# Kernel tuning notes

Hardware: AMD Instinct MI355X
Metric: run time of the kernel (lower is better)

Reference implementation:

```python
import jax, jax.numpy as jnp
import numpy as np

HID = 128
NUM_LAYERS = 3
B = 256
ND, ED, SD = 16384, 65536, 131072
NP_, EP, SP = 131072, 524288, 524288


def setup_inputs():
    key = jax.random.key(0)
    ks = jax.random.split(key, 40)
    r = lambda i, sh: jax.random.normal(ks[i], sh, jnp.float32) * 0.05
    ri = lambda i, sh, hi: jax.random.randint(ks[i], sh, 0, hi, jnp.int32)
    return {
        'drug_x': r(0, (ND, 78)),
        'prot_x': r(1, (NP_, 70)),
        'd_feature': r(2, (B, HID)),
        'p_feature': r(3, (B, HID)),
        'drug_edge_index': ri(4, (2, ED), ND),
        'drug_batch': jnp.sort(ri(5, (ND,), B)),
        'drug_sub_node': ri(6, (SD,), ND),
        'drug_sub_ind': ri(7, (SD,), ND),
        'prot_edge_index': ri(8, (2, EP), NP_),
        'prot_batch': jnp.sort(ri(9, (NP_,), B)),
        'prot_sub_node': ri(10, (SP,), NP_),
        'prot_sub_ind': ri(11, (SP,), NP_),
        'enc_Wd': r(12, (78, HID)), 'enc_bd': r(13, (HID,)),
        'enc_Wp': r(14, (70, HID)), 'enc_bp': r(15, (HID,)),
        'convW_d': r(16, (NUM_LAYERS, HID, HID)), 'convb_d': r(17, (NUM_LAYERS, HID)),
        'convW_p': r(18, (NUM_LAYERS, HID, HID)), 'convb_p': r(19, (NUM_LAYERS, HID)),
        'bng_d': jnp.ones((NUM_LAYERS, HID), jnp.float32), 'bnb_d': jnp.zeros((NUM_LAYERS, HID), jnp.float32),
        'bng_p': jnp.ones((NUM_LAYERS, HID), jnp.float32), 'bnb_p': jnp.zeros((NUM_LAYERS, HID), jnp.float32),
        'vn_emb_d': r(20, (HID,)), 'vn_emb_p': r(21, (HID,)),
        'vnW_d': r(22, (NUM_LAYERS - 1, HID, HID)), 'vnb_d': r(23, (NUM_LAYERS - 1, HID)),
        'vnW_p': r(24, (NUM_LAYERS - 1, HID, HID)), 'vnb_p': r(25, (NUM_LAYERS - 1, HID)),
        'mlpd1_W': r(26, (2 * HID, HID)), 'mlpd1_b': r(27, (HID,)),
        'mlpd1_g': jnp.ones((HID,), jnp.float32), 'mlpd1_be': jnp.zeros((HID,), jnp.float32),
        'mlpp1_W': r(28, (2 * HID, HID)), 'mlpp1_b': r(29, (HID,)),
        'mlpp1_g': jnp.ones((HID,), jnp.float32), 'mlpp1_be': jnp.zeros((HID,), jnp.float32),
    }


def _bn(x, g, b):
    # training-mode batch norm (batch statistics)
    m = jnp.mean(x, 0)
    v = jnp.var(x, 0)
    return (x - m) * jax.lax.rsqrt(v + 1e-5) * g + b


def _seg_mean(x, ids, n):
    s = jax.ops.segment_sum(x, ids, num_segments=n)
    c = jax.ops.segment_sum(jnp.ones((x.shape[0],), x.dtype), ids, num_segments=n)
    return s / jnp.maximum(c, 1.0)[:, None]


def _gcn(h, W, b, ei, n):
    # PyG GCNConv: sym-normalized A+I, then linear
    src, dst = ei[0], ei[1]
    hw = h @ W
    deg = jax.ops.segment_sum(jnp.ones((src.shape[0],), h.dtype), dst, num_segments=n) + 1.0
    nrm = jax.lax.rsqrt(deg)
    msg = hw[src] * (nrm[src] * nrm[dst])[:, None]  # [E, HID]
    return jax.ops.segment_sum(msg, dst, num_segments=n) + hw * (nrm * nrm)[:, None] + b


def _forward(fl, ints):
    (drug_x, prot_x, d_feature, p_feature, enc_Wd, enc_bd, enc_Wp, enc_bp,
     convW_d, convb_d, convW_p, convb_p, bng_d, bnb_d, bng_p, bnb_p,
     vn_emb_d, vn_emb_p, vnW_d, vnb_d, vnW_p, vnb_p,
     mlpd1_W, mlpd1_b, mlpd1_g, mlpd1_be, mlpp1_W, mlpp1_b, mlpp1_g, mlpp1_be) = fl
    (d_ei, d_batch, d_sn, d_si, p_ei, p_batch, p_sn, p_si) = ints
    Nd, Npn = drug_x.shape[0], prot_x.shape[0]
    Bn = d_feature.shape[0]
    hd = drug_x @ enc_Wd + enc_bd
    hp = prot_x @ enc_Wp + enc_bp
    # virtual node init: learned embedding + pretrained fingerprint feature
    vx_d = vn_emb_d[None, :] + d_feature  # [B, HID]
    vx_p = vn_emb_p[None, :] + p_feature
    for i in range(NUM_LAYERS):
        # virtual-node broadcast -> GCN -> BN -> ReLU (dropout off / eval)
        hd = _gcn(hd + vx_d[d_batch], convW_d[i], convb_d[i], d_ei, Nd)
        hp = _gcn(hp + vx_p[p_batch], convW_p[i], convb_p[i], p_ei, Npn)
        hd = jax.nn.relu(_bn(hd, bng_d[i], bnb_d[i]))
        hp = jax.nn.relu(_bn(hp, bng_p[i], bnb_p[i]))
        # k-hop subgraph structure extraction (scatter_mean back to nodes)
        hd_struct = _seg_mean(hd[d_sn], d_si, Nd)
        hp_struct = _seg_mean(hp[p_sn], p_si, Npn)
        if i < NUM_LAYERS - 1:
            vx_d = vx_d + jax.nn.relu((jax.ops.segment_sum(hd_struct, d_batch, num_segments=Bn) + vx_d) @ vnW_d[i] + vnb_d[i])
            vx_p = vx_p + jax.nn.relu((jax.ops.segment_sum(hp_struct, p_batch, num_segments=Bn) + vx_p) @ vnW_p[i] + vnb_p[i])
    # cross-modal sync: broadcast pooled drug info onto protein nodes & vice versa
    sync_drug = hp_struct + _seg_mean(hd_struct, d_batch, Bn)[p_batch]  # [Np, HID]
    sync_prot = hd_struct + _seg_mean(hp_struct, p_batch, Bn)[d_batch]  # [Nd, HID]
    final_drug = _bn(jnp.concatenate([_seg_mean(sync_prot, d_batch, Bn), d_feature], 1) @ mlpd1_W + mlpd1_b, mlpd1_g, mlpd1_be)
    final_prot = _bn(jnp.concatenate([_seg_mean(sync_drug, p_batch, Bn), p_feature], 1) @ mlpp1_W + mlpp1_b, mlpp1_g, mlpp1_be)
    return final_drug, final_prot


def reference(drug_x, prot_x, d_feature, p_feature, drug_edge_index, drug_batch,
              drug_sub_node, drug_sub_ind, prot_edge_index, prot_batch,
              prot_sub_node, prot_sub_ind, enc_Wd, enc_bd, enc_Wp, enc_bp,
              convW_d, convb_d, convW_p, convb_p, bng_d, bnb_d, bng_p, bnb_p,
              vn_emb_d, vn_emb_p, vnW_d, vnb_d, vnW_p, vnb_p,
              mlpd1_W, mlpd1_b, mlpd1_g, mlpd1_be, mlpp1_W, mlpp1_b, mlpp1_g, mlpp1_be):
    fl = (drug_x, prot_x, d_feature, p_feature, enc_Wd, enc_bd, enc_Wp, enc_bp,
          convW_d, convb_d, convW_p, convb_p, bng_d, bnb_d, bng_p, bnb_p,
          vn_emb_d, vn_emb_p, vnW_d, vnb_d, vnW_p, vnb_p,
          mlpd1_W, mlpd1_b, mlpd1_g, mlpd1_be, mlpp1_W, mlpp1_b, mlpp1_g, mlpp1_be)
    ints = (drug_edge_index, drug_batch, drug_sub_node, drug_sub_ind,
            prot_edge_index, prot_batch, prot_sub_node, prot_sub_ind)
    return _forward(fl, ints)
```

## Files before the change

### kernel.cpp

```cpp
#include <hip/hip_runtime.h>
#include <cstdint>
#include <cstddef>

#define HID 128
#define HB 1024

using bf16x8 = __attribute__((ext_vector_type(8))) short;
using f32x4v = __attribute__((ext_vector_type(4))) float;

static __device__ __forceinline__ unsigned short f2b(float x) {
  unsigned int u = __float_as_uint(x);
  unsigned int r = u + 0x7FFFu + ((u >> 16) & 1u);
  return (unsigned short)(r >> 16);
}
static __device__ __forceinline__ float b2f(unsigned short h) {
  return __uint_as_float(((unsigned int)h) << 16);
}
static __device__ __forceinline__ float4 b2f4(ushort4 h) {
  return make_float4(b2f(h.x), b2f(h.y), b2f(h.z), b2f(h.w));
}

static __device__ __forceinline__ int lowerb(const int* __restrict__ a, int n, int v) {
  int lo = 0, hi = n;
  while (lo < hi) { int m = (lo + hi) >> 1; if (a[m] < v) lo = m + 1; else hi = m; }
  return lo;
}

__global__ __launch_bounds__(256)
void k_prep1(const int* p_dst, int EP, int* deg_p, const int* d_dst, int ED, int* deg_d,
             const int* p_si, int SP, int* scnt_p, const int* d_si, int SD, int* scnt_d,
             const float* convW_d, const float* convW_p,
             const float* enc_Wd, const float* enc_Wp,
             unsigned short* WhiAll, unsigned short* WloAll,
             const float* emb_d, const float* d_feat, float* vx_d,
             const float* emb_p, const float* p_feat, float* vx_p, int vhalf) {
  const int b = blockIdx.x;
  const int tid = threadIdx.x;
  if (b < 4 * HB) {
    const int seg = b & 3, lb = b >> 2;
    const int stride = HB * 256;
    const int* idx = seg == 0 ? p_dst : seg == 1 ? d_dst : seg == 2 ? p_si : d_si;
    int* cnt = seg == 0 ? deg_p : seg == 1 ? deg_d : seg == 2 ? scnt_p : scnt_d;
    const int n = seg == 0 ? EP : seg == 1 ? ED : seg == 2 ? SP : SD;
    for (int i = lb * 256 + tid; i < n; i += stride) atomicAdd(&cnt[idx[i]], 1);
  } else if (b < 4 * HB + 256) {
    const int lb = b - 4 * HB;
    const int seg = lb >> 5;
    const float* W;
    int K;
    if (seg < 3) { W = convW_d + (size_t)seg * HID * HID; K = 128; }
    else if (seg < 6) { W = convW_p + (size_t)(seg - 3) * HID * HID; K = 128; }
    else if (seg == 6) { W = enc_Wd; K = 78; }
    else { W = enc_Wp; K = 70; }
    unsigned short* Whi = WhiAll + (size_t)seg * HID * HID;
    unsigned short* Wlo = WloAll + (size_t)seg * HID * HID;
    for (int i = (lb & 31) * 256 + tid; i < HID * HID; i += 32 * 256) {
      const int c = i >> 7, k = i & 127;
      const float v = (k < K) ? W[k * HID + c] : 0.f;
      const unsigned short hi = f2b(v);
      Whi[i] = hi;
      Wlo[i] = f2b(v - b2f(hi));
    }
  } else {
    const int lb = b - (4 * HB + 256);
    for (int i = lb * 256 + tid; i < 2 * vhalf; i += 128 * 256) {
      if (i < vhalf) vx_d[i] = emb_d[i & (HID - 1)] + d_feat[i];
      else { const int j = i - vhalf; vx_p[j] = emb_p[j & (HID - 1)] + p_feat[j]; }
    }
  }
}

__global__ void k_nrm_nb(const int* deg_d, float* nrm_d, int ND,
                         const int* deg_p, float* nrm_p, int NP,
                         const int* d_batch, float* nb_d,
                         const int* p_batch, float* nb_p, int B) {
  const int stride = gridDim.x * blockDim.x;
  const int total = ND + NP + 2 * B;
  for (int i = blockIdx.x * blockDim.x + threadIdx.x; i < total; i += stride) {
    if (i < ND) nrm_d[i] = rsqrtf((float)deg_d[i] + 1.0f);
    else if (i < ND + NP) { const int j = i - ND; nrm_p[j] = rsqrtf((float)deg_p[j] + 1.0f); }
    else if (i < ND + NP + B) {
      const int b = i - ND - NP;
      nb_d[b] = (float)(lowerb(d_batch, ND, b + 1) - lowerb(d_batch, ND, b));
    } else {
      const int b = i - ND - NP - B;
      nb_p[b] = (float)(lowerb(p_batch, NP, b + 1) - lowerb(p_batch, NP, b));
    }
  }
}

__global__ __launch_bounds__(256)
void k_scan1_all(const int* c0, int* r0, int n0, int nb0,
                 const int* c1, int* r1, int n1, int nb1,
                 const int* c2, int* r2, int n2, int nb2,
                 const int* c3, int* r3, int n3, int nb3, int* aux) {
  __shared__ int sh[256];
  int b = blockIdx.x, seg = 0;
  if (b >= nb0) { b -= nb0; seg = 1; }
  if (seg == 1 && b >= nb1) { b -= nb1; seg = 2; }
  if (seg == 2 && b >= nb2) { b -= nb2; seg = 3; }
  const int* cnt = seg == 0 ? c0 : seg == 1 ? c1 : seg == 2 ? c2 : c3;
  int* row = seg == 0 ? r0 : seg == 1 ? r1 : seg == 2 ? r2 : r3;
  const int n = seg == 0 ? n0 : seg == 1 ? n1 : seg == 2 ? n2 : n3;
  const int tid = threadIdx.x;
  const int base = b * 1024 + tid * 4;
  int v0 = base + 0 < n ? cnt[base + 0] : 0;
  int v1 = base + 1 < n ? cnt[base + 1] : 0;
  int v2 = base + 2 < n ? cnt[base + 2] : 0;
  int v3 = base + 3 < n ? cnt[base + 3] : 0;
  const int s = v0 + v1 + v2 + v3;
  sh[tid] = s;
  __syncthreads();
  for (int o = 1; o < 256; o <<= 1) {
    const int t = (tid >= o) ? sh[tid - o] : 0;
    __syncthreads();
    sh[tid] += t;
    __syncthreads();
  }
  int excl = sh[tid] - s;
  if (tid == 255) aux[seg * 256 + b] = sh[255];
  if (base + 0 < n) row[base + 0] = excl; excl += v0;
  if (base + 1 < n) row[base + 1] = excl; excl += v1;
  if (base + 2 < n) row[base + 2] = excl; excl += v2;
  if (base + 3 < n) row[base + 3] = excl;
}

__global__ __launch_bounds__(256)
void k_scan2_all(int* aux, int nb0, int nb1, int nb2, int nb3) {
  __shared__ int sh[256];
  const int seg = blockIdx.x;
  const int nb = seg == 0 ? nb0 : seg == 1 ? nb1 : seg == 2 ? nb2 : nb3;
  int* a = aux + seg * 256;
  const int tid = threadIdx.x;
  const int v = tid < nb ? a[tid] : 0;
  sh[tid] = v;
  __syncthreads();
  for (int o = 1; o < 256; o <<= 1) {
    const int t = (tid >= o) ? sh[tid - o] : 0;
    __syncthreads();
    sh[tid] += t;
    __syncthreads();
  }
  if (tid < nb) a[tid] = sh[tid] - v;
}

__global__ __launch_bounds__(256)
void k_scan3_all(int* r0, int n0, int nb0, int t0, int* r1, int n1, int nb1, int t1,
                 int* r2, int n2, int nb2, int t2, int* r3, int n3, int nb3, int t3,
                 const int* aux) {
  int b = blockIdx.x, seg = 0;
  if (b >= nb0) { b -= nb0; seg = 1; }
  if (seg == 1 && b >= nb1) { b -= nb1; seg = 2; }
  if (seg == 2 && b >= nb2) { b -= nb2; seg = 3; }
  int* row = seg == 0 ? r0 : seg == 1 ? r1 : seg == 2 ? r2 : r3;
  const int n = seg == 0 ? n0 : seg == 1 ? n1 : seg == 2 ? n2 : n3;
  const int total = seg == 0 ? t0 : seg == 1 ? t1 : seg == 2 ? t2 : t3;
  const int add = aux[seg * 256 + b];
  const int base = b * 1024 + threadIdx.x * 4;
  #pragma unroll
  for (int k = 0; k < 4; ++k)
    if (base + k < n) row[base + k] += add;
  if (b == 0 && threadIdx.x == 0) row[n] = total;
}

__global__ void k_fill_all(const int* p_src, const int* p_dst, const int* rowE_p, int* curE_p,
                           int* colE_p, int EP,
                           const int* d_src, const int* d_dst, const int* rowE_d, int* curE_d,
                           int* colE_d, int ED,
                           const int* p_sn, const int* p_si, const int* rowS_p, int* curS_p,
                           int* colS_p, int SP,
                           const int* d_sn, const int* d_si, const int* rowS_d, int* curS_d,
                           int* colS_d, int SD) {
  const int seg = blockIdx.x & 3;
  const int lb = blockIdx.x >> 2;
  const int stride = (gridDim.x >> 2) * blockDim.x;
  const int start = lb * blockDim.x + threadIdx.x;
  if (seg == 0) {
    for (int e = start; e < EP; e += stride) {
      const int d = p_dst[e];
      colE_p[rowE_p[d] + atomicAdd(&curE_p[d], 1)] = p_src[e];
    }
  } else if (seg == 1) {
    for (int e = start; e < ED; e += stride) {
      const int d = d_dst[e];
      colE_d[rowE_d[d] + atomicAdd(&curE_d[d], 1)] = d_src[e];
    }
  } else if (seg == 2) {
    for (int j = start; j < SP; j += stride) {
      const int t = p_si[j];
      colS_p[rowS_p[t] + atomicAdd(&curS_p[t], 1)] = p_sn[j];
    }
  } else {
    for (int j = start; j < SD; j += stride) {
      const int t = d_si[j];
      colS_d[rowS_d[t] + atomicAdd(&curS_d[t], 1)] = d_sn[j];
    }
  }
}

__global__ __launch_bounds__(256, 2)
void k_gemm_both(const unsigned short* Zhi0, const unsigned short* Zlo0,
                 const unsigned short* Whi0, const unsigned short* Wlo0,
                 unsigned short* G0, int nbk0,
                 const unsigned short* Zhi1, const unsigned short* Zlo1,
                 const unsigned short* Whi1, const unsigned short* Wlo1,
                 unsigned short* G1, float* stats_sl) {
  __shared__ unsigned short Bt[128 * 132];
  __shared__ float lstats[256];
  const int bid = blockIdx.x;
  const bool isP = bid >= nbk0;
  const int lb = isP ? bid - nbk0 : bid;
  const unsigned short* Zhi = isP ? Zhi1 : Zhi0;
  const unsigned short* Zlo = isP ? Zlo1 : Zlo0;
  const unsigned short* Wthi = isP ? Whi1 : Whi0;
  const unsigned short* Wtlo = isP ? Wlo1 : Wlo0;
  unsigned short* G = isP ? G1 : G0;
  const int slice = (isP ? 32 : 0) + (lb & 31);

  const int tid = threadIdx.x;
  const int w = tid >> 6;
  const int l = tid & 63;
  const int l15 = l & 15;
  const int kb = l >> 4;

  for (int i = tid; i < 128 * 16; i += 256) {
    const int c = i >> 4, k8 = i & 15;
    *(bf16x8*)(&Bt[c * 132 + k8 * 8]) = *(const bf16x8*)(Wthi + (size_t)c * 128 + k8 * 8);
  }
  lstats[tid] = 0.f;

  const int rbase = lb * 128 + w * 32 + l15;
  bf16x8 ahi[2][4], alo[2][4];
  #pragma unroll
  for (int rt = 0; rt < 2; ++rt)
    #pragma unroll
    for (int ks = 0; ks < 4; ++ks) {
      ahi[rt][ks] = *(const bf16x8*)(Zhi + (size_t)(rbase + rt * 16) * 128 + ks * 32 + kb * 8);
      alo[rt][ks] = *(const bf16x8*)(Zlo + (size_t)(rbase + rt * 16) * 128 + ks * 32 + kb * 8);
    }

  f32x4v acc[2][8];
  #pragma unroll
  for (int rt = 0; rt < 2; ++rt)
    #pragma unroll
    for (int ct = 0; ct < 8; ++ct)
      acc[rt][ct] = (f32x4v){0.f, 0.f, 0.f, 0.f};

  __syncthreads();
  #pragma unroll
  for (int ks = 0; ks < 4; ++ks) {
    #pragma unroll
    for (int ct = 0; ct < 8; ++ct) {
      const bf16x8 b = *(const bf16x8*)(&Bt[(ct * 16 + l15) * 132 + ks * 32 + kb * 8]);
      acc[0][ct] = __builtin_amdgcn_mfma_f32_16x16x32_bf16(ahi[0][ks], b, acc[0][ct], 0, 0, 0);
      acc[1][ct] = __builtin_amdgcn_mfma_f32_16x16x32_bf16(ahi[1][ks], b, acc[1][ct], 0, 0, 0);
      acc[0][ct] = __builtin_amdgcn_mfma_f32_16x16x32_bf16(alo[0][ks], b, acc[0][ct], 0, 0, 0);
      acc[1][ct] = __builtin_amdgcn_mfma_f32_16x16x32_bf16(alo[1][ks], b, acc[1][ct], 0, 0, 0);
    }
  }
  __syncthreads();

  for (int i = tid; i < 128 * 16; i += 256) {
    const int c = i >> 4, k8 = i & 15;
    *(bf16x8*)(&Bt[c * 132 + k8 * 8]) = *(const bf16x8*)(Wtlo + (size_t)c * 128 + k8 * 8);
  }
  __syncthreads();
  #pragma unroll
  for (int ks = 0; ks < 4; ++ks) {
    #pragma unroll
    for (int ct = 0; ct < 8; ++ct) {
      const bf16x8 b = *(const bf16x8*)(&Bt[(ct * 16 + l15) * 132 + ks * 32 + kb * 8]);
      acc[0][ct] = __builtin_amdgcn_mfma_f32_16x16x32_bf16(ahi[0][ks], b, acc[0][ct], 0, 0, 0);
      acc[1][ct] = __builtin_amdgcn_mfma_f32_16x16x32_bf16(ahi[1][ks], b, acc[1][ct], 0, 0, 0);
    }
  }

  float csum[8], csq[8];
  #pragma unroll
  for (int ct = 0; ct < 8; ++ct) { csum[ct] = 0.f; csq[ct] = 0.f; }
  #pragma unroll
  for (int rt = 0; rt < 2; ++rt) {
    const size_t grow = (size_t)lb * 128 + w * 32 + rt * 16 + (l >> 4) * 4;
    #pragma unroll
    for (int j = 0; j < 4; ++j) {
      unsigned short* gr = G + (grow + j) * 128 + l15;
      #pragma unroll
      for (int ct = 0; ct < 8; ++ct) {
        const float v = acc[rt][ct][j];
        gr[ct * 16] = f2b(v);
        csum[ct] += v;
        csq[ct] += v * v;
      }
    }
  }
  #pragma unroll
  for (int ct = 0; ct < 8; ++ct) {
    csum[ct] += __shfl_xor(csum[ct], 16);
    csum[ct] += __shfl_xor(csum[ct], 32);
    csq[ct] += __shfl_xor(csq[ct], 16);
    csq[ct] += __shfl_xor(csq[ct], 32);
  }
  if (l < 16) {
    #pragma unroll
    for (int ct = 0; ct < 8; ++ct) {
      atomicAdd(&lstats[ct * 16 + l], csum[ct]);
      atomicAdd(&lstats[128 + ct * 16 + l], csq[ct]);
    }
  }
  __syncthreads();
  atomicAdd(&stats_sl[(size_t)slice * 256 + tid], lstats[tid]);
}

__global__ __launch_bounds__(256, 2)
void k_gemm_enc_direct(const float* X0, int K0,
                       const unsigned short* Whi0, const unsigned short* Wlo0,
                       const float* bias0, unsigned short* G0, int nbk0,
                       const float* X1, int K1,
                       const unsigned short* Whi1, const unsigned short* Wlo1,
                       const float* bias1, unsigned short* G1) {
  __shared__ unsigned short Bt[128 * 132];
  const int bid = blockIdx.x;
  const bool isP = bid >= nbk0;
  const int lb = isP ? bid - nbk0 : bid;
  const float* X = isP ? X1 : X0;
  const int K = isP ? K1 : K0;
  const unsigned short* Wthi = isP ? Whi1 : Whi0;
  const unsigned short* Wtlo = isP ? Wlo1 : Wlo0;
  const float* bias = isP ? bias1 : bias0;
  unsigned short* G = isP ? G1 : G0;

  const int tid = threadIdx.x;
  const int w = tid >> 6;
  const int l = tid & 63;
  const int l15 = l & 15;
  const int kb = l >> 4;

  for (int i = tid; i < 128 * 16; i += 256) {
    const int c = i >> 4, k8 = i & 15;
    *(bf16x8*)(&Bt[c * 132 + k8 * 8]) = *(const bf16x8*)(Wthi + (size_t)c * 128 + k8 * 8);
  }

  const int rbase = lb * 128 + w * 32 + l15;
  bf16x8 ahi[2][4], alo[2][4];
  #pragma unroll
  for (int rt = 0; rt < 2; ++rt) {
    const float* xr = X + (size_t)(rbase + rt * 16) * K;
    #pragma unroll
    for (int ks = 0; ks < 4; ++ks) {
      #pragma unroll
      for (int j = 0; j < 8; ++j) {
        const int k = ks * 32 + kb * 8 + j;
        const float v = (k < K) ? xr[k] : 0.f;
        const unsigned short hi = f2b(v);
        ahi[rt][ks][j] = (short)hi;
        alo[rt][ks][j] = (short)f2b(v - b2f(hi));
      }
    }
  }

  f32x4v acc[2][8];
  #pragma unroll
  for (int rt = 0; rt < 2; ++rt)
    #pragma unroll
    for (int ct = 0; ct < 8; ++ct)
      acc[rt][ct] = (f32x4v){0.f, 0.f, 0.f, 0.f};

  __syncthreads();
  #pragma unroll
  for (int ks = 0; ks < 4; ++ks) {
    #pragma unroll
    for (int ct = 0; ct < 8; ++ct) {
      const bf16x8 b = *(const bf16x8*)(&Bt[(ct * 16 + l15) * 132 + ks * 32 + kb * 8]);
      acc[0][ct] = __builtin_amdgcn_mfma_f32_16x16x32_bf16(ahi[0][ks], b, acc[0][ct], 0, 0, 0);
      acc[1][ct] = __builtin_amdgcn_mfma_f32_16x16x32_bf16(ahi[1][ks], b, acc[1][ct], 0, 0, 0);
      acc[0][ct] = __builtin_amdgcn_mfma_f32_16x16x32_bf16(alo[0][ks], b, acc[0][ct], 0, 0, 0);
      acc[1][ct] = __builtin_amdgcn_mfma_f32_16x16x32_bf16(alo[1][ks], b, acc[1][ct], 0, 0, 0);
    }
  }
  __syncthreads();

  for (int i = tid; i < 128 * 16; i += 256) {
    const int c = i >> 4, k8 = i & 15;
    *(bf16x8*)(&Bt[c * 132 + k8 * 8]) = *(const bf16x8*)(Wtlo + (size_t)c * 128 + k8 * 8);
  }
  __syncthreads();
  #pragma unroll
  for (int ks = 0; ks < 4; ++ks) {
    #pragma unroll
    for (int ct = 0; ct < 8; ++ct) {
      const bf16x8 b = *(const bf16x8*)(&Bt[(ct * 16 + l15) * 132 + ks * 32 + kb * 8]);
      acc[0][ct] = __builtin_amdgcn_mfma_f32_16x16x32_bf16(ahi[0][ks], b, acc[0][ct], 0, 0, 0);
      acc[1][ct] = __builtin_amdgcn_mfma_f32_16x16x32_bf16(ahi[1][ks], b, acc[1][ct], 0, 0, 0);
    }
  }

  float bb[8];
  #pragma unroll
  for (int ct = 0; ct < 8; ++ct) bb[ct] = bias[ct * 16 + l15];
  #pragma unroll
  for (int rt = 0; rt < 2; ++rt) {
    const size_t grow = (size_t)lb * 128 + w * 32 + rt * 16 + (l >> 4) * 4;
    #pragma unroll
    for (int j = 0; j < 4; ++j) {
      unsigned short* gr = G + (grow + j) * 128 + l15;
      #pragma unroll
      for (int ct = 0; ct < 8; ++ct)
        gr[ct * 16] = f2b(acc[rt][ct][j] + bb[ct]);
    }
  }
}

__global__ __launch_bounds__(128)
void k_bn_scale_both(float* __restrict__ stats_sl,
                     const float* g0, const float* b0, float invN0, float* scsh0, float* zero0,
                     const float* g1, const float* b1, float invN1, float* scsh1, float* zero1,
                     int zn4) {
  const int seg = blockIdx.x;
  float* base = stats_sl + (size_t)seg * 32 * 256;
  const float* g = seg ? g1 : g0;
  const float* bb = seg ? b1 : b0;
  const float invN = seg ? invN1 : invN0;
  float* scsh = seg ? scsh1 : scsh0;
  float* zero = seg ? zero1 : zero0;
  const int c = threadIdx.x;
  float s = 0.f, ss = 0.f;
  for (int k = 0; k < 32; ++k) {
    s += base[(size_t)k * 256 + c];
    ss += base[(size_t)k * 256 + 128 + c];
    base[(size_t)k * 256 + c] = 0.f;
    base[(size_t)k * 256 + 128 + c] = 0.f;
  }
  const float m = s * invN;
  const float var = ss * invN - m * m;
  const float sc = g[c] * rsqrtf(var + 1e-5f);
  scsh[c] = sc;
  scsh[HID + c] = bb[c] - m * sc;
  const float4 z = {0.f, 0.f, 0.f, 0.f};
  for (int i = c; i < zn4; i += 128) ((float4*)zero)[i] = z;
}

template<bool HASF>
__global__ __launch_bounds__(256)
void k_agg_both(const int* rE0, const int* cE0, const unsigned short* G0,
                const float* scsh0, const int* bat0, const float* vx0, const float* nrm0,
                unsigned short* Zhi0, unsigned short* Zlo0, int nbk0,
                const int* rE1, const int* cE1, const unsigned short* G1,
                const float* scsh1, const int* bat1, const float* vx1, const float* nrm1,
                unsigned short* Zhi1, unsigned short* Zlo1) {
  const int bid = blockIdx.x;
  const bool isP = bid >= nbk0;
  const int lb = isP ? bid - nbk0 : bid;
  const int* rowp = isP ? rE1 : rE0;
  const int* colp = isP ? cE1 : cE0;
  const unsigned short* G = isP ? G1 : G0;
  const float* scsh = isP ? scsh1 : scsh0;
  const int* batch = isP ? bat1 : bat0;
  const float* vx = isP ? vx1 : vx0;
  const float* nrm = isP ? nrm1 : nrm0;
  unsigned short* Zhi = isP ? Zhi1 : Zhi0;
  unsigned short* Zlo = isP ? Zlo1 : Zlo0;

  const int tid = threadIdx.x;
  const int node = lb * 8 + (tid >> 5);
  const int c4 = tid & 31;
  float4 sc, shv;
  if constexpr (HASF) {
    sc = ((const float4*)scsh)[c4];
    shv = ((const float4*)(scsh + HID))[c4];
  }
  auto loadU = [&](int i) -> float4 {
    float4 v = b2f4(*(const ushort4*)(G + (size_t)i * HID + c4 * 4));
    if constexpr (HASF) {
      v.x = fmaxf(v.x * sc.x + shv.x, 0.f);
      v.y = fmaxf(v.y * sc.y + shv.y, 0.f);
      v.z = fmaxf(v.z * sc.z + shv.z, 0.f);
      v.w = fmaxf(v.w * sc.w + shv.w, 0.f);
    }
    const float4 u = *(const float4*)(vx + (size_t)batch[i] * HID + c4 * 4);
    v.x += u.x; v.y += u.y; v.z += u.z; v.w += u.w;
    return v;
  };
  const int lo = rowp[node], hi = rowp[node + 1];
  const float nv = nrm[node];
  const float s2 = nv * nv;
  float4 acc = loadU(node);
  acc.x *= s2; acc.y *= s2; acc.z *= s2; acc.w *= s2;
  int e = lo;
  for (; e + 4 <= hi; e += 4) {
    const int i0 = colp[e], i1 = colp[e + 1], i2 = colp[e + 2], i3 = colp[e + 3];
    const float w0 = nrm[i0] * nv, w1 = nrm[i1] * nv, w2 = nrm[i2] * nv, w3 = nrm[i3] * nv;
    const float4 v0 = loadU(i0);
    const float4 v1 = loadU(i1);
    const float4 v2 = loadU(i2);
    const float4 v3 = loadU(i3);
    acc.x += v0.x * w0 + v1.x * w1 + v2.x * w2 + v3.x * w3;
    acc.y += v0.y * w0 + v1.y * w1 + v2.y * w2 + v3.y * w3;
    acc.z += v0.z * w0 + v1.z * w1 + v2.z * w2 + v3.z * w3;
    acc.w += v0.w * w0 + v1.w * w1 + v2.w * w2 + v3.w * w3;
  }
  for (; e < hi; ++e) {
    const int i0 = colp[e];
    const float w = nrm[i0] * nv;
    const float4 v = loadU(i0);
    acc.x += v.x * w; acc.y += v.y * w; acc.z += v.z * w; acc.w += v.w * w;
  }
  ushort4 h, lo4;
  h.x = f2b(acc.x); lo4.x = f2b(acc.x - b2f(h.x));
  h.y = f2b(acc.y); lo4.y = f2b(acc.y - b2f(h.y));
  h.z = f2b(acc.z); lo4.z = f2b(acc.z - b2f(h.z));
  h.w = f2b(acc.w); lo4.w = f2b(acc.w - b2f(h.w));
  *(ushort4*)(Zhi + (size_t)node * HID + c4 * 4) = h;
  *(ushort4*)(Zlo + (size_t)node * HID + c4 * 4) = lo4;
}

__global__ __launch_bounds__(256)
void k_sub_pool_both(const int* rS0, const int* cS0, const unsigned short* G0, const float* scsh0,
                     const int* bat0, float* sumS0, int nbk0,
                     const int* rS1, const int* cS1, const unsigned short* G1, const float* scsh1,
                     const int* bat1, float* sumS1) {
  __shared__ float sh[8][HID];
  __shared__ int batl[8];
  const int bid = blockIdx.x;
  const bool isP = bid >= nbk0;
  const int lb = isP ? bid - nbk0 : bid;
  const int* rowp = isP ? rS1 : rS0;
  const int* colp = isP ? cS1 : cS0;
  const unsigned short* G = isP ? G1 : G0;
  const float* scsh = isP ? scsh1 : scsh0;
  const int* batch = isP ? bat1 : bat0;
  float* sumS = isP ? sumS1 : sumS0;

  const int tid = threadIdx.x;
  const int grp = tid >> 5;
  const int node = lb * 8 + grp;
  const int c4 = tid & 31;
  const float4 sc = ((const float4*)scsh)[c4];
  const float4 shv = ((const float4*)(scsh + HID))[c4];
  const int lo = rowp[node], hi = rowp[node + 1];
  float4 acc = {0.f, 0.f, 0.f, 0.f};
  int e = lo;
  for (; e + 4 <= hi; e += 4) {
    const int i0 = colp[e], i1 = colp[e + 1], i2 = colp[e + 2], i3 = colp[e + 3];
    const float4 v0 = b2f4(*(const ushort4*)(G + (size_t)i0 * HID + c4 * 4));
    const float4 v1 = b2f4(*(const ushort4*)(G + (size_t)i1 * HID + c4 * 4));
    const float4 v2 = b2f4(*(const ushort4*)(G + (size_t)i2 * HID + c4 * 4));
    const float4 v3 = b2f4(*(const ushort4*)(G + (size_t)i3 * HID + c4 * 4));
    acc.x += fmaxf(v0.x * sc.x + shv.x, 0.f) + fmaxf(v1.x * sc.x + shv.x, 0.f)
           + fmaxf(v2.x * sc.x + shv.x, 0.f) + fmaxf(v3.x * sc.x + shv.x, 0.f);
    acc.y += fmaxf(v0.y * sc.y + shv.y, 0.f) + fmaxf(v1.y * sc.y + shv.y, 0.f)
           + fmaxf(v2.y * sc.y + shv.y, 0.f) + fmaxf(v3.y * sc.y + shv.y, 0.f);
    acc.z += fmaxf(v0.z * sc.z + shv.z, 0.f) + fmaxf(v1.z * sc.z + shv.z, 0.f)
           + fmaxf(v2.z * sc.z + shv.z, 0.f) + fmaxf(v3.z * sc.z + shv.z, 0.f);
    acc.w += fmaxf(v0.w * sc.w + shv.w, 0.f) + fmaxf(v1.w * sc.w + shv.w, 0.f)
           + fmaxf(v2.w * sc.w + shv.w, 0.f) + fmaxf(v3.w * sc.w + shv.w, 0.f);
  }
  for (; e < hi; ++e) {
    const float4 v = b2f4(*(const ushort4*)(G + (size_t)colp[e] * HID + c4 * 4));
    acc.x += fmaxf(v.x * sc.x + shv.x, 0.f);
    acc.y += fmaxf(v.y * sc.y + shv.y, 0.f);
    acc.z += fmaxf(v.z * sc.z + shv.z, 0.f);
    acc.w += fmaxf(v.w * sc.w + shv.w, 0.f);
  }
  const float inv = 1.0f / fmaxf((float)(hi - lo), 1.0f);
  acc.x *= inv; acc.y *= inv; acc.z *= inv; acc.w *= inv;
  ((float4*)&sh[grp][0])[c4] = acc;
  if (tid < 8) batl[tid] = batch[lb * 8 + tid];
  __syncthreads();
  if (tid < HID) {
    int cur = batl[0];
    float a = 0.f;
    #pragma unroll
    for (int g = 0; g < 8; ++g) {
      if (batl[g] != cur) {
        atomicAdd(&sumS[(size_t)cur * HID + tid], a);
        a = 0.f;
        cur = batl[g];
      }
      a += sh[g][tid];
    }
    atomicAdd(&sumS[(size_t)cur * HID + tid], a);
  }
}

__global__ __launch_bounds__(128)
void k_vn_update_both(const float* ps0, float* vx0, const float* W0, const float* b0,
                      const float* ps1, float* vx1, const float* W1, const float* b1, int B) {
  const int gb = blockIdx.x;
  const bool isP = gb >= B;
  const int b = isP ? gb - B : gb;
  const float* pooledSum = isP ? ps1 : ps0;
  float* vx = isP ? vx1 : vx0;
  const float* W = isP ? W1 : W0;
  const float* bias = isP ? b1 : b0;
  const int c = threadIdx.x;
  __shared__ float xin[HID];
  xin[c] = pooledSum[(size_t)b * HID + c] + vx[(size_t)b * HID + c];
  __syncthreads();
  float acc = bias[c];
  #pragma unroll 8
  for (int k = 0; k < HID; k += 4) {
    const float4 x = *(const float4*)&xin[k];
    acc += x.x * W[k * HID + c] + x.y * W[(k + 1) * HID + c]
         + x.z * W[(k + 2) * HID + c] + x.w * W[(k + 3) * HID + c];
  }
  vx[(size_t)b * HID + c] += fmaxf(acc, 0.0f);
}

__global__ __launch_bounds__(128)
void k_final_A(const float* __restrict__ sum_Sd, const float* __restrict__ sum_Sp,
               const float* __restrict__ nb_d, const float* __restrict__ nb_p,
               float* __restrict__ A_d, float* __restrict__ A_p) {
  const int b = blockIdx.x, c = threadIdx.x;
  const float nd = nb_d[b], np_ = nb_p[b];
  const float md = sum_Sd[(size_t)b * HID + c] / fmaxf(nd, 1.f);
  const float mp = sum_Sp[(size_t)b * HID + c] / fmaxf(np_, 1.f);
  A_d[(size_t)b * HID + c] = md + (nd > 0.f ? mp : 0.f);
  A_p[(size_t)b * HID + c] = mp + (np_ > 0.f ? md : 0.f);
}

__global__ __launch_bounds__(128)
void k_final_mlp_both(const float* A0, const float* f0, const float* W0, const float* b0,
                      const float* A1, const float* f1, const float* W1, const float* b1,
                      float* __restrict__ fpre, int B) {
  const int gb = blockIdx.x;
  const bool isP = gb >= B;
  const int b = isP ? gb - B : gb;
  const float* A = isP ? A1 : A0;
  const float* feat = isP ? f1 : f0;
  const float* W = isP ? W1 : W0;
  const float* bias = isP ? b1 : b0;
  const int c = threadIdx.x;
  __shared__ float xin[2 * HID];
  xin[c] = A[(size_t)b * HID + c];
  xin[HID + c] = feat[(size_t)b * HID + c];
  __syncthreads();
  float acc = bias[c];
  #pragma unroll 8
  for (int k = 0; k < 2 * HID; k += 4) {
    const float4 x = *(const float4*)&xin[k];
    acc += x.x * W[k * HID + c] + x.y * W[(k + 1) * HID + c]
         + x.z * W[(k + 2) * HID + c] + x.w * W[(k + 3) * HID + c];
  }
  fpre[(size_t)gb * HID + c] = acc;
}

__global__ __launch_bounds__(256)
void k_bn_stats_both(const float* __restrict__ fpre, float* __restrict__ statsF, int B) {
  __shared__ float sh[2][256];
  const int seg = blockIdx.x >= 128 ? 1 : 0;
  const int lb = blockIdx.x - seg * 128;
  const float* X = fpre + (size_t)seg * B * HID;
  float* stats = statsF + seg * 256;
  const int tid = threadIdx.x;
  const int c = tid & (HID - 1);
  const int half = tid >> 7;
  float s = 0.f, ss = 0.f;
  for (int r = lb * 2 + half; r < B; r += 256) {
    const float v = X[(size_t)r * HID + c];
    s += v; ss += v * v;
  }
  sh[0][tid] = s; sh[1][tid] = ss;
  __syncthreads();
  if (tid < HID) {
    atomicAdd(&stats[c], sh[0][tid] + sh[0][tid + 128]);
    atomicAdd(&stats[HID + c], sh[1][tid] + sh[1][tid + 128]);
  }
}

__global__ void k_bn_apply_both(const float* __restrict__ fpre, float* __restrict__ out,
                                const float* __restrict__ statsF,
                                const float* g0, const float* b0,
                                const float* g1, const float* b1, int B, float invN) {
  const int stride = gridDim.x * blockDim.x;
  const int n4 = 2 * B * 32;
  for (int i = blockIdx.x * blockDim.x + threadIdx.x; i < n4; i += stride) {
    const int seg = i >= B * 32 ? 1 : 0;
    const int c4 = i & 31;
    const float* stats = statsF + seg * 256;
    const float4 m4 = ((const float4*)stats)[c4];
    const float4 q4 = ((const float4*)stats)[32 + c4];
    const float4 g4 = ((const float4*)(seg ? g1 : g0))[c4];
    const float4 b4 = ((const float4*)(seg ? b1 : b0))[c4];
    float4 v = ((const float4*)fpre)[i];
    float m, va;
    m = m4.x * invN; va = q4.x * invN - m * m; v.x = (v.x - m) * rsqrtf(va + 1e-5f) * g4.x + b4.x;
    m = m4.y * invN; va = q4.y * invN - m * m; v.y = (v.y - m) * rsqrtf(va + 1e-5f) * g4.y + b4.y;
    m = m4.z * invN; va = q4.z * invN - m * m; v.z = (v.z - m) * rsqrtf(va + 1e-5f) * g4.z + b4.z;
    m = m4.w * invN; va = q4.w * invN - m * m; v.w = (v.w - m) * rsqrtf(va + 1e-5f) * g4.w + b4.w;
    ((float4*)out)[i] = v;
  }
}

extern "C" void kernel_launch(void* const* d_in, const int* in_sizes, int n_in,
                              void* d_out, int out_size, void* d_ws, size_t ws_size,
                              hipStream_t stream) {
  const float* drug_x   = (const float*)d_in[0];
  const float* prot_x   = (const float*)d_in[1];
  const float* d_feat   = (const float*)d_in[2];
  const float* p_feat   = (const float*)d_in[3];
  const int*   d_ei     = (const int*)d_in[4];
  const int*   d_batch  = (const int*)d_in[5];
  const int*   d_sn     = (const int*)d_in[6];
  const int*   d_si     = (const int*)d_in[7];
  const int*   p_ei     = (const int*)d_in[8];
  const int*   p_batch  = (const int*)d_in[9];
  const int*   p_sn     = (const int*)d_in[10];
  const int*   p_si     = (const int*)d_in[11];
  const float* enc_Wd   = (const float*)d_in[12];
  const float* enc_bd   = (const float*)d_in[13];
  const float* enc_Wp   = (const float*)d_in[14];
  const float* enc_bp   = (const float*)d_in[15];
  const float* convW_d  = (const float*)d_in[16];
  const float* convW_p  = (const float*)d_in[18];
  const float* bng_d    = (const float*)d_in[20];
  const float* bnb_d    = (const float*)d_in[21];
  const float* bng_p    = (const float*)d_in[22];
  const float* bnb_p    = (const float*)d_in[23];
  const float* vn_emb_d = (const float*)d_in[24];
  const float* vn_emb_p = (const float*)d_in[25];
  const float* vnW_d    = (const float*)d_in[26];
  const float* vnb_d    = (const float*)d_in[27];
  const float* vnW_p    = (const float*)d_in[28];
  const float* vnb_p    = (const float*)d_in[29];
  const float* mlpd1_W  = (const float*)d_in[30];
  const float* mlpd1_b  = (const float*)d_in[31];
  const float* mlpd1_g  = (const float*)d_in[32];
  const float* mlpd1_be = (const float*)d_in[33];
  const float* mlpp1_W  = (const float*)d_in[34];
  const float* mlpp1_b  = (const float*)d_in[35];
  const float* mlpp1_g  = (const float*)d_in[36];
  const float* mlpp1_be = (const float*)d_in[37];

  const int ND = in_sizes[5];
  const int ED = in_sizes[4] / 2;
  const int SD = in_sizes[6];
  const int NP = in_sizes[9];
  const int EP = in_sizes[8] / 2;
  const int SP = in_sizes[10];
  const int B  = in_sizes[2] / HID;
  (void)n_in; (void)out_size; (void)ws_size;

  char* wsb = (char*)d_ws;
  size_t off = 0;
  auto alloc = [&](size_t bytes) -> void* {
    void* p = (void*)(wsb + off);
    off = (off + bytes + 255) & ~(size_t)255;
    return p;
  };
  unsigned short* Gp = (unsigned short*)alloc((size_t)NP * HID * 2);
  unsigned short* Zhi_p = (unsigned short*)alloc((size_t)NP * HID * 2);
  unsigned short* Zlo_p = (unsigned short*)alloc((size_t)NP * HID * 2);
  unsigned short* Gd = (unsigned short*)alloc((size_t)ND * HID * 2);
  unsigned short* Zhi_d = (unsigned short*)alloc((size_t)ND * HID * 2);
  unsigned short* Zlo_d = (unsigned short*)alloc((size_t)ND * HID * 2);
  unsigned short* WhiAll = (unsigned short*)alloc((size_t)8 * HID * HID * 2);
  unsigned short* WloAll = (unsigned short*)alloc((size_t)8 * HID * HID * 2);
  float* nrm_p = (float*)alloc((size_t)NP * 4);
  float* nrm_d = (float*)alloc((size_t)ND * 4);
  int* rowE_p = (int*)alloc((size_t)(NP + 1) * 4);
  int* rowE_d = (int*)alloc((size_t)(ND + 1) * 4);
  int* rowS_p = (int*)alloc((size_t)(NP + 1) * 4);
  int* rowS_d = (int*)alloc((size_t)(ND + 1) * 4);
  int* colE_p = (int*)alloc((size_t)EP * 4);
  int* colE_d = (int*)alloc((size_t)ED * 4);
  int* colS_p = (int*)alloc((size_t)SP * 4);
  int* colS_d = (int*)alloc((size_t)SD * 4);
  int* aux    = (int*)alloc(4 * 256 * 4);
  float* vx_d  = (float*)alloc((size_t)B * HID * 4);
  float* vx_p  = (float*)alloc((size_t)B * HID * 4);
  float* sum_Sd = (float*)alloc((size_t)B * HID * 4);
  float* sum_Sp = (float*)alloc((size_t)B * HID * 4);
  float* A_d   = (float*)alloc((size_t)B * HID * 4);
  float* A_p   = (float*)alloc((size_t)B * HID * 4);
  float* nb_d  = (float*)alloc((size_t)B * 4);
  float* nb_p  = (float*)alloc((size_t)B * 4);
  float* scsh_d = (float*)alloc(2 * HID * 4);
  float* scsh_p = (float*)alloc(2 * HID * 4);
  float* fpre  = (float*)alloc((size_t)2 * B * HID * 4);
  float* statsF = (float*)alloc(2 * 256 * 4);
  const size_t zstart = off;
  int* deg_p  = (int*)alloc((size_t)NP * 4);
  int* deg_d  = (int*)alloc((size_t)ND * 4);
  int* scnt_p = (int*)alloc((size_t)NP * 4);
  int* scnt_d = (int*)alloc((size_t)ND * 4);
  int* curE_p = (int*)alloc((size_t)NP * 4);
  int* curE_d = (int*)alloc((size_t)ND * 4);
  int* curS_p = (int*)alloc((size_t)NP * 4);
  int* curS_d = (int*)alloc((size_t)ND * 4);
  float* stats_sl = (float*)alloc((size_t)64 * 256 * 4);
  const size_t zend = off;

  const int* d_src = d_ei;  const int* d_dst = d_ei + ED;
  const int* p_src = p_ei;  const int* p_dst = p_ei + EP;

  hipMemsetAsync(wsb + zstart, 0, zend - zstart, stream);
  k_prep1<<<4 * HB + 256 + 128, 256, 0, stream>>>(
      p_dst, EP, deg_p, d_dst, ED, deg_d, p_si, SP, scnt_p, d_si, SD, scnt_d,
      convW_d, convW_p, enc_Wd, enc_Wp, WhiAll, WloAll,
      vn_emb_d, d_feat, vx_d, vn_emb_p, p_feat, vx_p, B * HID);
  k_nrm_nb<<<1024, 256, 0, stream>>>(deg_d, nrm_d, ND, deg_p, nrm_p, NP,
                                     d_batch, nb_d, p_batch, nb_p, B);
  const int nbP = (NP + 1023) / 1024, nbD = (ND + 1023) / 1024;
  k_scan1_all<<<2 * nbP + 2 * nbD, 256, 0, stream>>>(
      deg_p, rowE_p, NP, nbP, deg_d, rowE_d, ND, nbD,
      scnt_p, rowS_p, NP, nbP, scnt_d, rowS_d, ND, nbD, aux);
  k_scan2_all<<<4, 256, 0, stream>>>(aux, nbP, nbD, nbP, nbD);
  k_scan3_all<<<2 * nbP + 2 * nbD, 256, 0, stream>>>(
      rowE_p, NP, nbP, EP, rowE_d, ND, nbD, ED,
      rowS_p, NP, nbP, SP, rowS_d, ND, nbD, SD, aux);
  k_fill_all<<<4096, 256, 0, stream>>>(
      p_src, p_dst, rowE_p, curE_p, colE_p, EP,
      d_src, d_dst, rowE_d, curE_d, colE_d, ED,
      p_sn, p_si, rowS_p, curS_p, colS_p, SP,
      d_sn, d_si, rowS_d, curS_d, colS_d, SD);

  k_gemm_enc_direct<<<ND / 128 + NP / 128, 256, 0, stream>>>(
      drug_x, 78, WhiAll + (size_t)6 * HID * HID, WloAll + (size_t)6 * HID * HID,
      enc_bd, Gd, ND / 128,
      prot_x, 70, WhiAll + (size_t)7 * HID * HID, WloAll + (size_t)7 * HID * HID,
      enc_bp, Gp);

  for (int l = 0; l < 3; ++l) {
    if (l == 0)
      k_agg_both<false><<<ND / 8 + NP / 8, 256, 0, stream>>>(
          rowE_d, colE_d, Gd, nullptr, d_batch, vx_d, nrm_d, Zhi_d, Zlo_d, ND / 8,
          rowE_p, colE_p, Gp, nullptr, p_batch, vx_p, nrm_p, Zhi_p, Zlo_p);
    else
      k_agg_both<true><<<ND / 8 + NP / 8, 256, 0, stream>>>(
          rowE_d, colE_d, Gd, scsh_d, d_batch, vx_d, nrm_d, Zhi_d, Zlo_d, ND / 8,
          rowE_p, colE_p, Gp, scsh_p, p_batch, vx_p, nrm_p, Zhi_p, Zlo_p);
    k_gemm_both<<<ND / 128 + NP / 128, 256, 0, stream>>>(
        Zhi_d, Zlo_d, WhiAll + (size_t)l * HID * HID, WloAll + (size_t)l * HID * HID,
        Gd, ND / 128,
        Zhi_p, Zlo_p, WhiAll + (size_t)(3 + l) * HID * HID, WloAll + (size_t)(3 + l) * HID * HID,
        Gp, stats_sl);
    k_bn_scale_both<<<2, 128, 0, stream>>>(stats_sl,
        bng_d + l * HID, bnb_d + l * HID, 1.0f / (float)ND, scsh_d, sum_Sd,
        bng_p + l * HID, bnb_p + l * HID, 1.0f / (float)NP, scsh_p, sum_Sp,
        B * HID / 4);
    k_sub_pool_both<<<ND / 8 + NP / 8, 256, 0, stream>>>(
        rowS_d, colS_d, Gd, scsh_d, d_batch, sum_Sd, ND / 8,
        rowS_p, colS_p, Gp, scsh_p, p_batch, sum_Sp);
    if (l < 2)
      k_vn_update_both<<<2 * B, 128, 0, stream>>>(
          sum_Sd, vx_d, vnW_d + (size_t)l * HID * HID, vnb_d + l * HID,
          sum_Sp, vx_p, vnW_p + (size_t)l * HID * HID, vnb_p + l * HID, B);
  }

  k_final_A<<<B, 128, 0, stream>>>(sum_Sd, sum_Sp, nb_d, nb_p, A_d, A_p);
  k_final_mlp_both<<<2 * B, 128, 0, stream>>>(A_d, d_feat, mlpd1_W, mlpd1_b,
                                              A_p, p_feat, mlpp1_W, mlpp1_b, fpre, B);
  hipMemsetAsync(statsF, 0, 2 * 256 * 4, stream);
  k_bn_stats_both<<<256, 256, 0, stream>>>(fpre, statsF, B);
  k_bn_apply_both<<<128, 256, 0, stream>>>(fpre, (float*)d_out, statsF,
                                           mlpd1_g, mlpd1_be, mlpp1_g, mlpp1_be,
                                           B, 1.0f / (float)B);
}
```

Before: 628.7 us.

## Partition histogram and CSR fill atomics by XCD node range; fuse final mean into MLP

The degree-count and CSR-fill kernels now map each block to one of eight XCDs by its low block-index bits. Each block only handles keys in that XCD's slice of the node range, so atomics on a given counter stay within one XCD's L2 and avoid cross-XCD coherence traffic. In exchange every XCD group re-reads the full index arrays, and the grids are smaller. Separately, the k_final_A kernel is folded into k_final_mlp_both, which removes one launch and the A_d/A_p buffers.

```diff
diff --git a/kernel.cpp b/kernel.cpp
--- a/kernel.cpp
+++ b/kernel.cpp
@@ -3,7 +3,6 @@
 #include <cstddef>
 
 #define HID 128
-#define HB 1024
 
 using bf16x8 = __attribute__((ext_vector_type(8))) short;
 using f32x4v = __attribute__((ext_vector_type(4))) float;
@@ -29,6 +28,7 @@
 __global__ __launch_bounds__(256)
 void k_prep1(const int* p_dst, int EP, int* deg_p, const int* d_dst, int ED, int* deg_d,
              const int* p_si, int SP, int* scnt_p, const int* d_si, int SD, int* scnt_d,
+             int NP, int ND,
              const float* convW_d, const float* convW_p,
              const float* enc_Wd, const float* enc_Wp,
              unsigned short* WhiAll, unsigned short* WloAll,
@@ -36,15 +36,25 @@
              const float* emb_p, const float* p_feat, float* vx_p, int vhalf) {
   const int b = blockIdx.x;
   const int tid = threadIdx.x;
-  if (b < 4 * HB) {
-    const int seg = b & 3, lb = b >> 2;
-    const int stride = HB * 256;
+  if (b < 1024) {
+    const int xcd = b & 7;
+    const int rest = b >> 3;
+    const int seg = rest & 3;
+    const int lb = rest >> 2;
+    const int stride = 32 * 256;
     const int* idx = seg == 0 ? p_dst : seg == 1 ? d_dst : seg == 2 ? p_si : d_si;
     int* cnt = seg == 0 ? deg_p : seg == 1 ? deg_d : seg == 2 ? scnt_p : scnt_d;
     const int n = seg == 0 ? EP : seg == 1 ? ED : seg == 2 ? SP : SD;
-    for (int i = lb * 256 + tid; i < n; i += stride) atomicAdd(&cnt[idx[i]], 1);
-  } else if (b < 4 * HB + 256) {
-    const int lb = b - 4 * HB;
+    const int nn = (seg == 0 || seg == 2) ? NP : ND;
+    const int chunk = (nn + 7) >> 3;
+    const int rlo = xcd * chunk;
+    const int rhi = min(nn, rlo + chunk);
+    for (int i = lb * 256 + tid; i < n; i += stride) {
+      const int v = idx[i];
+      if (v >= rlo && v < rhi) atomicAdd(&cnt[v], 1);
+    }
+  } else if (b < 1024 + 256) {
+    const int lb = b - 1024;
     const int seg = lb >> 5;
     const float* W;
     int K;
@@ -62,7 +72,7 @@
       Wlo[i] = f2b(v - b2f(hi));
     }
   } else {
-    const int lb = b - (4 * HB + 256);
+    const int lb = b - (1024 + 256);
     for (int i = lb * 256 + tid; i < 2 * vhalf; i += 128 * 256) {
       if (i < vhalf) vx_d[i] = emb_d[i & (HID - 1)] + d_feat[i];
       else { const int j = i - vhalf; vx_p[j] = emb_p[j & (HID - 1)] + p_feat[j]; }
@@ -170,31 +180,28 @@
                            const int* p_sn, const int* p_si, const int* rowS_p, int* curS_p,
                            int* colS_p, int SP,
                            const int* d_sn, const int* d_si, const int* rowS_d, int* curS_d,
-                           int* colS_d, int SD) {
-  const int seg = blockIdx.x & 3;
-  const int lb = blockIdx.x >> 2;
-  const int stride = (gridDim.x >> 2) * blockDim.x;
-  const int start = lb * blockDim.x + threadIdx.x;
-  if (seg == 0) {
-    for (int e = start; e < EP; e += stride) {
-      const int d = p_dst[e];
-      colE_p[rowE_p[d] + atomicAdd(&curE_p[d], 1)] = p_src[e];
-    }
-  } else if (seg == 1) {
-    for (int e = start; e < ED; e += stride) {
-      const int d = d_dst[e];
-      colE_d[rowE_d[d] + atomicAdd(&curE_d[d], 1)] = d_src[e];
-    }
-  } else if (seg == 2) {
-    for (int j = start; j < SP; j += stride) {
-      const int t = p_si[j];
-      colS_p[rowS_p[t] + atomicAdd(&curS_p[t], 1)] = p_sn[j];
-    }
-  } else {
-    for (int j = start; j < SD; j += stride) {
-      const int t = d_si[j];
-      colS_d[rowS_d[t] + atomicAdd(&curS_d[t], 1)] = d_sn[j];
-    }
+                           int* colS_d, int SD, int NP, int ND) {
+  const int b = blockIdx.x;
+  const int xcd = b & 7;
+  const int rest = b >> 3;
+  const int seg = rest & 3;
+  const int lb = rest >> 2;
+  const int stride = 64 * 256;
+  const int start = lb * 256 + threadIdx.x;
+  const int* key = seg == 0 ? p_dst : seg == 1 ? d_dst : seg == 2 ? p_si : d_si;
+  const int* val = seg == 0 ? p_src : seg == 1 ? d_src : seg == 2 ? p_sn : d_sn;
+  const int* row = seg == 0 ? rowE_p : seg == 1 ? rowE_d : seg == 2 ? rowS_p : rowS_d;
+  int* cur = seg == 0 ? curE_p : seg == 1 ? curE_d : seg == 2 ? curS_p : curS_d;
+  int* col = seg == 0 ? colE_p : seg == 1 ? colE_d : seg == 2 ? colS_p : colS_d;
+  const int n = seg == 0 ? EP : seg == 1 ? ED : seg == 2 ? SP : SD;
+  const int nn = (seg == 0 || seg == 2) ? NP : ND;
+  const int chunk = (nn + 7) >> 3;
+  const int rlo = xcd * chunk;
+  const int rhi = min(nn, rlo + chunk);
+  for (int i = start; i < n; i += stride) {
+    const int k = key[i];
+    if (k >= rlo && k < rhi)
+      col[row[k] + atomicAdd(&cur[k], 1)] = val[i];
   }
 }
 
@@ -607,31 +614,23 @@
 }
 
 __global__ __launch_bounds__(128)
-void k_final_A(const float* __restrict__ sum_Sd, const float* __restrict__ sum_Sp,
-               const float* __restrict__ nb_d, const float* __restrict__ nb_p,
-               float* __restrict__ A_d, float* __restrict__ A_p) {
-  const int b = blockIdx.x, c = threadIdx.x;
-  const float nd = nb_d[b], np_ = nb_p[b];
-  const float md = sum_Sd[(size_t)b * HID + c] / fmaxf(nd, 1.f);
-  const float mp = sum_Sp[(size_t)b * HID + c] / fmaxf(np_, 1.f);
-  A_d[(size_t)b * HID + c] = md + (nd > 0.f ? mp : 0.f);
-  A_p[(size_t)b * HID + c] = mp + (np_ > 0.f ? md : 0.f);
-}
-
-__global__ __launch_bounds__(128)
-void k_final_mlp_both(const float* A0, const float* f0, const float* W0, const float* b0,
-                      const float* A1, const float* f1, const float* W1, const float* b1,
+void k_final_mlp_both(const float* sum_Sd, const float* sum_Sp,
+                      const float* nb_d, const float* nb_p,
+                      const float* f0, const float* W0, const float* b0,
+                      const float* f1, const float* W1, const float* b1,
                       float* __restrict__ fpre, int B) {
   const int gb = blockIdx.x;
   const bool isP = gb >= B;
   const int b = isP ? gb - B : gb;
-  const float* A = isP ? A1 : A0;
   const float* feat = isP ? f1 : f0;
   const float* W = isP ? W1 : W0;
   const float* bias = isP ? b1 : b0;
   const int c = threadIdx.x;
   __shared__ float xin[2 * HID];
-  xin[c] = A[(size_t)b * HID + c];
+  const float nd = nb_d[b], np_ = nb_p[b];
+  const float md = sum_Sd[(size_t)b * HID + c] / fmaxf(nd, 1.f);
+  const float mp = sum_Sp[(size_t)b * HID + c] / fmaxf(np_, 1.f);
+  xin[c] = isP ? (mp + (np_ > 0.f ? md : 0.f)) : (md + (nd > 0.f ? mp : 0.f));
   xin[HID + c] = feat[(size_t)b * HID + c];
   __syncthreads();
   float acc = bias[c];
@@ -770,8 +769,6 @@
   float* vx_p  = (float*)alloc((size_t)B * HID * 4);
   float* sum_Sd = (float*)alloc((size_t)B * HID * 4);
   float* sum_Sp = (float*)alloc((size_t)B * HID * 4);
-  float* A_d   = (float*)alloc((size_t)B * HID * 4);
-  float* A_p   = (float*)alloc((size_t)B * HID * 4);
   float* nb_d  = (float*)alloc((size_t)B * 4);
   float* nb_p  = (float*)alloc((size_t)B * 4);
   float* scsh_d = (float*)alloc(2 * HID * 4);
@@ -794,8 +791,9 @@
   const int* p_src = p_ei;  const int* p_dst = p_ei + EP;
 
   hipMemsetAsync(wsb + zstart, 0, zend - zstart, stream);
-  k_prep1<<<4 * HB + 256 + 128, 256, 0, stream>>>(
+  k_prep1<<<1024 + 256 + 128, 256, 0, stream>>>(
       p_dst, EP, deg_p, d_dst, ED, deg_d, p_si, SP, scnt_p, d_si, SD, scnt_d,
+      NP, ND,
       convW_d, convW_p, enc_Wd, enc_Wp, WhiAll, WloAll,
       vn_emb_d, d_feat, vx_d, vn_emb_p, p_feat, vx_p, B * HID);
   k_nrm_nb<<<1024, 256, 0, stream>>>(deg_d, nrm_d, ND, deg_p, nrm_p, NP,
@@ -808,11 +806,11 @@
   k_scan3_all<<<2 * nbP + 2 * nbD, 256, 0, stream>>>(
       rowE_p, NP, nbP, EP, rowE_d, ND, nbD, ED,
       rowS_p, NP, nbP, SP, rowS_d, ND, nbD, SD, aux);
-  k_fill_all<<<4096, 256, 0, stream>>>(
+  k_fill_all<<<2048, 256, 0, stream>>>(
       p_src, p_dst, rowE_p, curE_p, colE_p, EP,
       d_src, d_dst, rowE_d, curE_d, colE_d, ED,
       p_sn, p_si, rowS_p, curS_p, colS_p, SP,
-      d_sn, d_si, rowS_d, curS_d, colS_d, SD);
+      d_sn, d_si, rowS_d, curS_d, colS_d, SD, NP, ND);
 
   k_gemm_enc_direct<<<ND / 128 + NP / 128, 256, 0, stream>>>(
       drug_x, 78, WhiAll + (size_t)6 * HID * HID, WloAll + (size_t)6 * HID * HID,
@@ -847,9 +845,9 @@
           sum_Sp, vx_p, vnW_p + (size_t)l * HID * HID, vnb_p + l * HID, B);
   }
 
-  k_final_A<<<B, 128, 0, stream>>>(sum_Sd, sum_Sp, nb_d, nb_p, A_d, A_p);
-  k_final_mlp_both<<<2 * B, 128, 0, stream>>>(A_d, d_feat, mlpd1_W, mlpd1_b,
-                                              A_p, p_feat, mlpp1_W, mlpp1_b, fpre, B);
+  k_final_mlp_both<<<2 * B, 128, 0, stream>>>(sum_Sd, sum_Sp, nb_d, nb_p,
+                                              d_feat, mlpd1_W, mlpd1_b,
+                                              p_feat, mlpp1_W, mlpp1_b, fpre, B);
   hipMemsetAsync(statsF, 0, 2 * 256 * 4, stream);
   k_bn_stats_both<<<256, 256, 0, stream>>>(fpre, statsF, B);
   k_bn_apply_both<<<128, 256, 0, stream>>>(fpre, (float*)d_out, statsF,
```

After: 633.7 us. Within noise of the previous version (+0.8%).
